# Kernel optimization log

Hardware: AMD Instinct MI355X
Metric: run time of the kernel (lower is better)

## Reference

```python
import jax, jax.numpy as jnp
import numpy as np
import math

B, T, D_IN, D_OUT = 4, 2048, 2048, 2048

def _inv_sigmoid(v):
    return math.log(v / (1 - v + 1e-08))

def setup_inputs() -> dict:
    key = jax.random.key(0)
    ks = jax.random.split(key, 6)
    x = jax.random.normal(ks[0], (B, T, D_IN), dtype=jnp.float32)
    W_p = jax.random.normal(ks[1], (D_OUT, D_IN), dtype=jnp.float32) * 0.02
    W_i = jax.random.normal(ks[2], (D_OUT, D_IN), dtype=jnp.float32) * 0.002
    W_d = jax.random.normal(ks[3], (D_OUT, D_IN), dtype=jnp.float32) * 0.002
    alpha_logit = jnp.full((D_IN,), _inv_sigmoid(0.9), dtype=jnp.float32)
    beta_logit = jnp.full((D_IN,), _inv_sigmoid(0.5), dtype=jnp.float32)
    W_gate_w = jax.random.normal(ks[4], (3, 3 * D_IN), dtype=jnp.float32) * 0.01
    W_gate_b = jnp.array([1.0, 0.0, 0.0], dtype=jnp.float32)
    bias = jnp.zeros((D_OUT,), dtype=jnp.float32)
    return {"x": x, "W_p": W_p, "W_i": W_i, "W_d": W_d,
            "alpha_logit": alpha_logit, "beta_logit": beta_logit,
            "W_gate_w": W_gate_w, "W_gate_b": W_gate_b, "bias": bias}

def _pid_features(x, alpha, beta):
    # x: (B,T,D). Single scan computing EMA integral and smoothed derivative.
    x_t = jnp.swapaxes(x, 0, 1)  # (T,B,D)
    x_prev = jnp.concatenate([jnp.zeros_like(x_t[:1]), x_t[:-1]], axis=0)
    diff_t = x_t - x_prev  # raw finite difference
    def step(carry, inp):
        s, d = carry
        xt, dt = inp
        s = alpha * s + (1.0 - alpha) * xt
        d = beta * d + (1.0 - beta) * dt
        return (s, d), (s, d)
    s0 = jnp.zeros(x.shape[::2], dtype=x.dtype)  # (B,D)
    _, (integ_t, deriv_t) = jax.lax.scan(step, (s0, s0), (x_t, diff_t))
    return jnp.swapaxes(integ_t, 0, 1), jnp.swapaxes(deriv_t, 0, 1)

def reference(x, W_p, W_i, W_d, alpha_logit, beta_logit, W_gate_w, W_gate_b, bias):
    alpha = jax.nn.sigmoid(alpha_logit)  # (D,)
    beta = jax.nn.sigmoid(beta_logit)
    integral, derivative = _pid_features(x, alpha, beta)  # (B,T,D) each
    gate_in = jnp.concatenate([x, integral, derivative], axis=-1)  # (B,T,3D)
    logits = jnp.einsum('btk,gk->btg', gate_in, W_gate_w) + W_gate_b
    gates = jax.nn.softmax(logits, axis=-1)  # (B,T,3)
    p_out = jnp.einsum('btd,od->bto', x, W_p)
    i_out = jnp.einsum('btd,od->bto', integral, W_i)
    d_out = jnp.einsum('btd,od->bto', derivative, W_d)
    y = gates[..., 0:1] * p_out + gates[..., 1:2] * i_out + gates[..., 2:3] * d_out + bias
    return y
```

## Files before the change

kernel.cpp:

```cpp
#include <hip/hip_runtime.h>
#include <stdint.h>

typedef unsigned short u16;

#define GAS __attribute__((address_space(1)))
#define LAS __attribute__((address_space(3)))

typedef __bf16 bf16x8 __attribute__((ext_vector_type(8)));
typedef float f32x4 __attribute__((ext_vector_type(4)));


__device__ inline u16 f2b(float f) {
    uint32_t x = __float_as_uint(f);
    uint32_t r = (x + 0x7fffu + ((x >> 16) & 1u)) >> 16;
    return (u16)r;
}

__device__ inline float b2f(u16 u) {
    union { uint32_t i; float f; } v;
    v.i = ((uint32_t)u) << 16;
    return v.f;
}

__device__ inline void load8b(float* v, const u16* p) {
    uint4 u = *(const uint4*)p;
    v[0] = b2f((u16)(u.x)); v[1] = b2f((u16)(u.x >> 16));
    v[2] = b2f((u16)(u.y)); v[3] = b2f((u16)(u.y >> 16));
    v[4] = b2f((u16)(u.z)); v[5] = b2f((u16)(u.z >> 16));
    v[6] = b2f((u16)(u.w)); v[7] = b2f((u16)(u.w >> 16));
}

__device__ inline void load8f(float* v, const float* p) {
    float4 a = *(const float4*)p;
    float4 b = *(const float4*)(p + 4);
    v[0] = a.x; v[1] = a.y; v[2] = a.z; v[3] = a.w;
    v[4] = b.x; v[5] = b.y; v[6] = b.z; v[7] = b.w;
}

__device__ inline void store8b(u16* p, const float* v, float scale) {
    uint4 u;
    u.x = (uint32_t)f2b(v[0] * scale) | ((uint32_t)f2b(v[1] * scale) << 16);
    u.y = (uint32_t)f2b(v[2] * scale) | ((uint32_t)f2b(v[3] * scale) << 16);
    u.z = (uint32_t)f2b(v[4] * scale) | ((uint32_t)f2b(v[5] * scale) << 16);
    u.w = (uint32_t)f2b(v[6] * scale) | ((uint32_t)f2b(v[7] * scale) << 16);
    *(uint4*)p = u;
}

__device__ inline float sigmoidf(float v) { return 1.f / (1.f + __expf(-v)); }

__device__ inline float pow64f(float a) {
    float p = a * a;
    p = p * p;
    p = p * p;
    p = p * p;
    p = p * p;
    return p * p;
}

__device__ inline float* carry_ptr(u16* Z, int plane, int b, int c, int d) {
    int f = ((plane * 4 + b) * 32 + c) * 2048 + d;
    int row = f >> 10;
    int off = f & 1023;
    return (float*)(Z + (size_t)row * 6144) + off;
}

__global__ __launch_bounds__(256) void pack_w(
    const float* __restrict__ Wp, const float* __restrict__ Wi,
    const float* __restrict__ Wd, u16* __restrict__ Wcat)
{
    int i = (blockIdx.x * 256 + threadIdx.x) * 8;
    int seg = i >> 22;
    int j = i & 4194303;
    const float* src = (seg == 0) ? Wp : (seg == 1) ? Wi : Wd;
    int o = j >> 11;
    int c = j & 2047;
    float v[8];
    load8f(v, src + j);
    store8b(Wcat + (size_t)o * 6144 + seg * 2048 + c, v, 1.0f);
}

__global__ __launch_bounds__(256) void scan_pass1(
    const float* __restrict__ x, const float* __restrict__ alog,
    const float* __restrict__ blog, u16* __restrict__ Z)
{
    const int d = blockIdx.x * 256 + threadIdx.x;
    const int c = blockIdx.y;
    const int b = blockIdx.z;
    const float alpha = sigmoidf(alog[d]);
    const float beta  = sigmoidf(blog[d]);
    const float oma = 1.f - alpha, omb = 1.f - beta;
    const float* xp = x + ((size_t)b * 2048 + c * 64) * 2048 + d;
    float xprev = (c == 0) ? 0.f : xp[-2048];
    float s = 0.f, dd = 0.f;
    #pragma unroll 8
    for (int t = 0; t < 64; ++t) {
        float xf = xp[(size_t)t * 2048];
        s = alpha * s + oma * xf;
        dd = beta * dd + omb * (xf - xprev);
        xprev = xf;
    }
    *carry_ptr(Z, 0, b, c, d) = s;
    *carry_ptr(Z, 1, b, c, d) = dd;
}

__global__ __launch_bounds__(256) void scan_pass2(
    const float* __restrict__ alog, const float* __restrict__ blog,
    u16* __restrict__ Z)
{
    const int g = blockIdx.x * 256 + threadIdx.x;
    const int b = g >> 11;
    const int d = g & 2047;
    const float aL = pow64f(sigmoidf(alog[d]));
    const float bL = pow64f(sigmoidf(blog[d]));
    float sIn = 0.f, dIn = 0.f;
    for (int c = 0; c < 32; ++c) {
        float* sp = carry_ptr(Z, 0, b, c, d);
        float* dp = carry_ptr(Z, 1, b, c, d);
        float sl = *sp, dl = *dp;
        *sp = sIn; *dp = dIn;
        sIn = sl + aL * sIn;
        dIn = dl + bL * dIn;
    }
}

__global__ __launch_bounds__(256) void scan_pass3(
    const float* __restrict__ x, const float* __restrict__ alog,
    const float* __restrict__ blog, u16* __restrict__ Z)
{
    const int d = blockIdx.x * 256 + threadIdx.x;
    const int c = blockIdx.y;
    const int b = blockIdx.z;
    const float alpha = sigmoidf(alog[d]);
    const float beta  = sigmoidf(blog[d]);
    const float oma = 1.f - alpha, omb = 1.f - beta;
    const float* xp = x + ((size_t)b * 2048 + c * 64) * 2048 + d;
    u16* zp = Z + ((size_t)b * 2048 + c * 64) * 6144 + 2048 + d;
    float s  = *carry_ptr(Z, 0, b, c, d);
    float dd = *carry_ptr(Z, 1, b, c, d);
    float xprev = (c == 0) ? 0.f : xp[-2048];
    #pragma unroll 8
    for (int t = 0; t < 64; ++t) {
        float xf = xp[(size_t)t * 2048];
        s = alpha * s + oma * xf;
        dd = beta * dd + omb * (xf - xprev);
        xprev = xf;
        size_t zo = (size_t)t * 6144;
        zp[zo] = f2b(s);
        zp[zo + 2048] = f2b(dd);
    }
}

__global__ __launch_bounds__(256) void gates_kernel(
    const float* __restrict__ x, const float* __restrict__ Wg,
    const float* __restrict__ Wgb, u16* __restrict__ Z)
{
    const int row = blockIdx.x;
    const int tid = threadIdx.x;
    const int k = tid * 8;
    const float* xr = x + (size_t)row * 2048;
    u16* zr = Z + (size_t)row * 6144;

    float xv[8], sv[8], dv[8];
    load8f(xv, xr + k);
    load8b(sv, zr + 2048 + k);
    load8b(dv, zr + 4096 + k);

    float p[3];
    #pragma unroll
    for (int gg = 0; gg < 3; ++gg) {
        float wx[8], ws[8], wd[8];
        load8f(wx, Wg + gg * 6144 + k);
        load8f(ws, Wg + gg * 6144 + 2048 + k);
        load8f(wd, Wg + gg * 6144 + 4096 + k);
        float acc = 0.f;
        #pragma unroll
        for (int j = 0; j < 8; ++j)
            acc += xv[j] * wx[j] + sv[j] * ws[j] + dv[j] * wd[j];
        p[gg] = acc;
    }

    #pragma unroll
    for (int off = 32; off > 0; off >>= 1) {
        p[0] += __shfl_down(p[0], off);
        p[1] += __shfl_down(p[1], off);
        p[2] += __shfl_down(p[2], off);
    }

    __shared__ float red[4][3];
    __shared__ float gsh[3];
    int wv = tid >> 6, lane = tid & 63;
    if (lane == 0) { red[wv][0] = p[0]; red[wv][1] = p[1]; red[wv][2] = p[2]; }
    __syncthreads();
    if (tid == 0) {
        float l0 = red[0][0] + red[1][0] + red[2][0] + red[3][0] + Wgb[0];
        float l1 = red[0][1] + red[1][1] + red[2][1] + red[3][1] + Wgb[1];
        float l2 = red[0][2] + red[1][2] + red[2][2] + red[3][2] + Wgb[2];
        float m = fmaxf(l0, fmaxf(l1, l2));
        float e0 = __expf(l0 - m), e1 = __expf(l1 - m), e2 = __expf(l2 - m);
        float inv = 1.f / (e0 + e1 + e2);
        gsh[0] = e0 * inv; gsh[1] = e1 * inv; gsh[2] = e2 * inv;
    }
    __syncthreads();
    float g0 = gsh[0], g1 = gsh[1], g2 = gsh[2];
    store8b(zr + k, xv, g0);
    store8b(zr + 2048 + k, sv, g1);
    store8b(zr + 4096 + k, dv, g2);
}

__global__ __launch_bounds__(512, 2) void gemm_kernel(
    const u16* __restrict__ Z, const u16* __restrict__ Wcat,
    const float* __restrict__ bias, float* __restrict__ out)
{
    extern __shared__ u16 lds[];
    u16* const lA = lds;
    u16* const lB = lds + 32768;

    const int tid = threadIdx.x;
    const int bn = blockIdx.x * 256;
    const int bm = blockIdx.y * 256;

    const int srow = tid >> 2;
    const int sgg  = (tid & 3) ^ ((tid >> 2) & 3) ^ ((tid >> 4) & 3);
    const u16* aglob = Z    + (size_t)(bm + srow) * 6144 + sgg * 8;
    const u16* bglob = Wcat + (size_t)(bn + srow) * 6144 + sgg * 8;

    const int lane = tid & 63;
    const int wv = tid >> 6;
    const int wm = wv & 1;
    const int wn = wv >> 1;
    const int fr = lane & 15;
    const int fq = lane >> 4;
    const int g  = fq ^ ((fr ^ (fr >> 2)) & 3);
    const int aoff = (wm * 128 + fr) * 32 + g * 8;
    const int boff = (wn * 64 + fr) * 32 + g * 8;

    f32x4 acc[8][4] = {};

#define XSTAGE(L, Gp, jt, h) do {                                             \
    u16* d_ = (L) + (((h) * 2 + ((jt) & 1)) * 8192) + tid * 8;                \
    const u16* s_ = (Gp) + (size_t)(jt) * 64 + (h) * 32;                      \
    __builtin_amdgcn_global_load_lds((const GAS uint32_t*)s_,                 \
                                     (LAS uint32_t*)d_, 16, 0, 0);            \
    __builtin_amdgcn_global_load_lds(                                         \
        (const GAS uint32_t*)(s_ + (size_t)128 * 6144),                       \
        (LAS uint32_t*)(d_ + 4096), 16, 0, 0);                                \
} while (0)

    XSTAGE(lA, aglob, 0, 0);
    XSTAGE(lB, bglob, 0, 0);
    XSTAGE(lA, aglob, 0, 1);
    XSTAGE(lB, bglob, 0, 1);
    XSTAGE(lA, aglob, 1, 0);
    XSTAGE(lB, bglob, 1, 0);
    asm volatile("s_waitcnt vmcnt(4)" ::: "memory");
    __builtin_amdgcn_s_barrier();

    for (int kt = 0; kt < 96; ++kt) {
        const int p = kt & 1;
        int t1 = kt + 1; if (t1 == 96) t1 = 0;
        int t2 = kt + 2; if (t2 >= 96) t2 -= 96;
        const u16* aLo = lA + (0 * 2 + p) * 8192;
        const u16* bLo = lB + (0 * 2 + p) * 8192;
        const u16* aHi = lA + (2 + p) * 8192;
        const u16* bHi = lB + (2 + p) * 8192;

        bf16x8 av[4], bv[4];

        #pragma unroll
        for (int i = 0; i < 4; ++i) av[i] = *(const bf16x8*)(aLo + aoff + i * 512);
        #pragma unroll
        for (int j = 0; j < 4; ++j) bv[j] = *(const bf16x8*)(bLo + boff + j * 512);
        XSTAGE(lA, aglob, t1, 1);
        __builtin_amdgcn_s_barrier();
        __builtin_amdgcn_s_setprio(1);
        #pragma unroll
        for (int i = 0; i < 4; ++i)
            #pragma unroll
            for (int j = 0; j < 4; ++j)
                acc[i][j] = __builtin_amdgcn_mfma_f32_16x16x32_bf16(
                    av[i], bv[j], acc[i][j], 0, 0, 0);
        __builtin_amdgcn_s_setprio(0);
        __builtin_amdgcn_s_barrier();

        #pragma unroll
        for (int i = 0; i < 4; ++i)
            av[i] = *(const bf16x8*)(aLo + aoff + (4 + i) * 512);
        XSTAGE(lB, bglob, t1, 1);
        __builtin_amdgcn_s_barrier();
        __builtin_amdgcn_s_setprio(1);
        #pragma unroll
        for (int i = 0; i < 4; ++i)
            #pragma unroll
            for (int j = 0; j < 4; ++j)
                acc[4 + i][j] = __builtin_amdgcn_mfma_f32_16x16x32_bf16(
                    av[i], bv[j], acc[4 + i][j], 0, 0, 0);
        __builtin_amdgcn_s_setprio(0);
        __builtin_amdgcn_s_barrier();

        #pragma unroll
        for (int i = 0; i < 4; ++i) av[i] = *(const bf16x8*)(aHi + aoff + i * 512);
        #pragma unroll
        for (int j = 0; j < 4; ++j) bv[j] = *(const bf16x8*)(bHi + boff + j * 512);
        XSTAGE(lA, aglob, t2, 0);
        __builtin_amdgcn_s_barrier();
        __builtin_amdgcn_s_setprio(1);
        #pragma unroll
        for (int i = 0; i < 4; ++i)
            #pragma unroll
            for (int j = 0; j < 4; ++j)
                acc[i][j] = __builtin_amdgcn_mfma_f32_16x16x32_bf16(
                    av[i], bv[j], acc[i][j], 0, 0, 0);
        __builtin_amdgcn_s_setprio(0);
        __builtin_amdgcn_s_barrier();

        #pragma unroll
        for (int i = 0; i < 4; ++i)
            av[i] = *(const bf16x8*)(aHi + aoff + (4 + i) * 512);
        XSTAGE(lB, bglob, t2, 0);
        __builtin_amdgcn_s_barrier();
        __builtin_amdgcn_s_setprio(1);
        #pragma unroll
        for (int i = 0; i < 4; ++i)
            #pragma unroll
            for (int j = 0; j < 4; ++j)
                acc[4 + i][j] = __builtin_amdgcn_mfma_f32_16x16x32_bf16(
                    av[i], bv[j], acc[4 + i][j], 0, 0, 0);
        __builtin_amdgcn_s_setprio(0);
        asm volatile("s_waitcnt vmcnt(4)" ::: "memory");
        __builtin_amdgcn_s_barrier();
    }

    asm volatile("s_waitcnt vmcnt(0)" ::: "memory");

    #pragma unroll
    for (int j = 0; j < 4; ++j) {
        const int col = bn + wn * 64 + j * 16 + fr;
        const float bb = bias[col];
        #pragma unroll
        for (int mf = 0; mf < 8; ++mf) {
            const int row0 = bm + wm * 128 + mf * 16 + fq * 4;
            #pragma unroll
            for (int r = 0; r < 4; ++r)
                out[(size_t)(row0 + r) * 2048 + col] = acc[mf][j][r] + bb;
        }
    }
#undef XSTAGE
}

extern "C" void kernel_launch(void* const* d_in, const int* in_sizes, int n_in,
                              void* d_out, int out_size, void* d_ws, size_t ws_size,
                              hipStream_t stream) {
    const float* x    = (const float*)d_in[0];
    const float* Wp   = (const float*)d_in[1];
    const float* Wi   = (const float*)d_in[2];
    const float* Wd   = (const float*)d_in[3];
    const float* al   = (const float*)d_in[4];
    const float* bl   = (const float*)d_in[5];
    const float* Wg   = (const float*)d_in[6];
    const float* Wgb  = (const float*)d_in[7];
    const float* bias = (const float*)d_in[8];
    float* out = (float*)d_out;

    u16* Z    = (u16*)d_ws;
    u16* Wcat = (u16*)((char*)d_ws + (size_t)8192 * 6144 * 2);

    static bool lds_cfgd = false;
    if (!lds_cfgd) {
        (void)hipFuncSetAttribute((const void*)gemm_kernel,
                                  hipFuncAttributeMaxDynamicSharedMemorySize,
                                  131072);
        lds_cfgd = true;
    }

    pack_w<<<6144, 256, 0, stream>>>(Wp, Wi, Wd, Wcat);
    scan_pass1<<<dim3(8, 32, 4), 256, 0, stream>>>(x, al, bl, Z);
    scan_pass2<<<32, 256, 0, stream>>>(al, bl, Z);
    scan_pass3<<<dim3(8, 32, 4), 256, 0, stream>>>(x, al, bl, Z);
    gates_kernel<<<8192, 256, 0, stream>>>(x, Wg, Wgb, Z);
    gemm_kernel<<<dim3(8, 32), 512, 131072, stream>>>(Z, Wcat, bias, out);
}
```

Baseline: 426.7 us.

## Restructure GEMM LDS staging to 64-wide K tiles with new swizzle

Changes the LDS tile layout from two 32-wide K halves to 64-element rows with an 8-way XOR swizzle. Each K-step now stages the full 64-wide K slice, split into row-quarter pieces, into a double buffer. The wait counts are adjusted so the next tile's global-to-LDS loads overlap the MFMA phases. This should cut bank conflicts and simplify the prefetch schedule, but the pipeline depth drops from two tiles ahead to one, which risks exposing memory latency. The last iteration redundantly reloads tile 95.

```diff
diff --git a/kernel.cpp b/kernel.cpp
--- a/kernel.cpp
+++ b/kernel.cpp
@@ -219,10 +219,10 @@
     const int bn = blockIdx.x * 256;
     const int bm = blockIdx.y * 256;
 
-    const int srow = tid >> 2;
-    const int sgg  = (tid & 3) ^ ((tid >> 2) & 3) ^ ((tid >> 4) & 3);
-    const u16* aglob = Z    + (size_t)(bm + srow) * 6144 + sgg * 8;
-    const u16* bglob = Wcat + (size_t)(bn + srow) * 6144 + sgg * 8;
+    const int sr  = tid >> 3;
+    const int scq = (tid & 7) ^ (sr & 7);
+    const u16* aglob = Z    + (size_t)(bm + sr) * 6144 + scq * 8;
+    const u16* bglob = Wcat + (size_t)(bn + sr) * 6144 + scq * 8;
 
     const int lane = tid & 63;
     const int wv = tid >> 6;
@@ -230,48 +230,46 @@
     const int wn = wv >> 1;
     const int fr = lane & 15;
     const int fq = lane >> 4;
-    const int g  = fq ^ ((fr ^ (fr >> 2)) & 3);
-    const int aoff = (wm * 128 + fr) * 32 + g * 8;
-    const int boff = (wn * 64 + fr) * 32 + g * 8;
+    const int chlo = fq ^ (fr & 7);
+    const int aoff = fr * 64 + chlo * 8;
+    const int boff = ((wn & 1) * 64 + fr) * 64 + chlo * 8;
+    const int aoffh = aoff ^ 32;
+    const int boffh = boff ^ 32;
 
     f32x4 acc[8][4] = {};
 
-#define XSTAGE(L, Gp, jt, h) do {                                             \
-    u16* d_ = (L) + (((h) * 2 + ((jt) & 1)) * 8192) + tid * 8;                \
-    const u16* s_ = (Gp) + (size_t)(jt) * 64 + (h) * 32;                      \
-    __builtin_amdgcn_global_load_lds((const GAS uint32_t*)s_,                 \
-                                     (LAS uint32_t*)d_, 16, 0, 0);            \
-    __builtin_amdgcn_global_load_lds(                                         \
-        (const GAS uint32_t*)(s_ + (size_t)128 * 6144),                       \
-        (LAS uint32_t*)(d_ + 4096), 16, 0, 0);                                \
-} while (0)
-
-    XSTAGE(lA, aglob, 0, 0);
-    XSTAGE(lB, bglob, 0, 0);
-    XSTAGE(lA, aglob, 0, 1);
-    XSTAGE(lB, bglob, 0, 1);
-    XSTAGE(lA, aglob, 1, 0);
-    XSTAGE(lB, bglob, 1, 0);
-    asm volatile("s_waitcnt vmcnt(4)" ::: "memory");
+#define GLOAD(gsrc, ldst)                                                     \
+    __builtin_amdgcn_global_load_lds((const GAS uint32_t*)(gsrc),             \
+                                     (LAS uint32_t*)(ldst), 16, 0, 0)
+
+    GLOAD(bglob,                        lB + tid * 8);
+    GLOAD(bglob + (size_t) 64 * 6144,   lB + 4096 + tid * 8);
+    GLOAD(bglob + (size_t)128 * 6144,   lB + 8192 + tid * 8);
+    GLOAD(bglob + (size_t)192 * 6144,   lB + 8192 + 4096 + tid * 8);
+    GLOAD(aglob,                        lA + tid * 8);
+    GLOAD(aglob + (size_t)128 * 6144,   lA + 8192 + tid * 8);
+    GLOAD(aglob + (size_t) 64 * 6144,   lA + 4096 + tid * 8);
+    GLOAD(aglob + (size_t)192 * 6144,   lA + 8192 + 4096 + tid * 8);
+    asm volatile("s_waitcnt vmcnt(2)" ::: "memory");
     __builtin_amdgcn_s_barrier();
 
     for (int kt = 0; kt < 96; ++kt) {
-        const int p = kt & 1;
-        int t1 = kt + 1; if (t1 == 96) t1 = 0;
-        int t2 = kt + 2; if (t2 >= 96) t2 -= 96;
-        const u16* aLo = lA + (0 * 2 + p) * 8192;
-        const u16* bLo = lB + (0 * 2 + p) * 8192;
-        const u16* aHi = lA + (2 + p) * 8192;
-        const u16* bHi = lB + (2 + p) * 8192;
-
+        const int pb  = (kt & 1) * 2;
+        const int nbb = pb ^ 2;
+        const int t1  = (kt < 95) ? kt + 1 : 95;
+        const size_t kc = (size_t)t1 * 64;
+        const u16* aS = lA + (pb + wm) * 8192;
+        const u16* bS = lB + (pb + (wn >> 1)) * 8192;
         bf16x8 av[4], bv[4];
 
         #pragma unroll
-        for (int i = 0; i < 4; ++i) av[i] = *(const bf16x8*)(aLo + aoff + i * 512);
-        #pragma unroll
-        for (int j = 0; j < 4; ++j) bv[j] = *(const bf16x8*)(bLo + boff + j * 512);
-        XSTAGE(lA, aglob, t1, 1);
-        __builtin_amdgcn_s_barrier();
+        for (int i = 0; i < 4; ++i) av[i] = *(const bf16x8*)(aS + aoff + i * 1024);
+        #pragma unroll
+        for (int j = 0; j < 4; ++j) bv[j] = *(const bf16x8*)(bS + boff + j * 1024);
+        GLOAD(bglob + kc,                      lB + nbb * 8192 + tid * 8);
+        GLOAD(bglob + (size_t)64 * 6144 + kc,  lB + nbb * 8192 + 4096 + tid * 8);
+        __builtin_amdgcn_s_barrier();
+        asm volatile("s_waitcnt lgkmcnt(0)" ::: "memory");
         __builtin_amdgcn_s_setprio(1);
         #pragma unroll
         for (int i = 0; i < 4; ++i)
@@ -280,13 +278,16 @@
                 acc[i][j] = __builtin_amdgcn_mfma_f32_16x16x32_bf16(
                     av[i], bv[j], acc[i][j], 0, 0, 0);
         __builtin_amdgcn_s_setprio(0);
-        __builtin_amdgcn_s_barrier();
-
-        #pragma unroll
-        for (int i = 0; i < 4; ++i)
-            av[i] = *(const bf16x8*)(aLo + aoff + (4 + i) * 512);
-        XSTAGE(lB, bglob, t1, 1);
-        __builtin_amdgcn_s_barrier();
+        asm volatile("s_waitcnt vmcnt(2)" ::: "memory");
+        __builtin_amdgcn_s_barrier();
+
+        #pragma unroll
+        for (int i = 0; i < 4; ++i)
+            av[i] = *(const bf16x8*)(aS + aoff + 4096 + i * 1024);
+        GLOAD(bglob + (size_t)128 * 6144 + kc, lB + (nbb + 1) * 8192 + tid * 8);
+        GLOAD(bglob + (size_t)192 * 6144 + kc, lB + (nbb + 1) * 8192 + 4096 + tid * 8);
+        __builtin_amdgcn_s_barrier();
+        asm volatile("s_waitcnt lgkmcnt(0)" ::: "memory");
         __builtin_amdgcn_s_setprio(1);
         #pragma unroll
         for (int i = 0; i < 4; ++i)
@@ -298,11 +299,13 @@
         __builtin_amdgcn_s_barrier();
 
         #pragma unroll
-        for (int i = 0; i < 4; ++i) av[i] = *(const bf16x8*)(aHi + aoff + i * 512);
-        #pragma unroll
-        for (int j = 0; j < 4; ++j) bv[j] = *(const bf16x8*)(bHi + boff + j * 512);
-        XSTAGE(lA, aglob, t2, 0);
-        __builtin_amdgcn_s_barrier();
+        for (int i = 0; i < 4; ++i) av[i] = *(const bf16x8*)(aS + aoffh + i * 1024);
+        #pragma unroll
+        for (int j = 0; j < 4; ++j) bv[j] = *(const bf16x8*)(bS + boffh + j * 1024);
+        GLOAD(aglob + kc,                      lA + nbb * 8192 + tid * 8);
+        GLOAD(aglob + (size_t)128 * 6144 + kc, lA + (nbb + 1) * 8192 + tid * 8);
+        __builtin_amdgcn_s_barrier();
+        asm volatile("s_waitcnt lgkmcnt(0)" ::: "memory");
         __builtin_amdgcn_s_setprio(1);
         #pragma unroll
         for (int i = 0; i < 4; ++i)
@@ -315,9 +318,11 @@
 
         #pragma unroll
         for (int i = 0; i < 4; ++i)
-            av[i] = *(const bf16x8*)(aHi + aoff + (4 + i) * 512);
-        XSTAGE(lB, bglob, t2, 0);
-        __builtin_amdgcn_s_barrier();
+            av[i] = *(const bf16x8*)(aS + aoffh + 4096 + i * 1024);
+        GLOAD(aglob + (size_t) 64 * 6144 + kc, lA + nbb * 8192 + 4096 + tid * 8);
+        GLOAD(aglob + (size_t)192 * 6144 + kc, lA + (nbb + 1) * 8192 + 4096 + tid * 8);
+        __builtin_amdgcn_s_barrier();
+        asm volatile("s_waitcnt lgkmcnt(0)" ::: "memory");
         __builtin_amdgcn_s_setprio(1);
         #pragma unroll
         for (int i = 0; i < 4; ++i)
@@ -326,7 +331,7 @@
                 acc[4 + i][j] = __builtin_amdgcn_mfma_f32_16x16x32_bf16(
                     av[i], bv[j], acc[4 + i][j], 0, 0, 0);
         __builtin_amdgcn_s_setprio(0);
-        asm volatile("s_waitcnt vmcnt(4)" ::: "memory");
+        asm volatile("s_waitcnt vmcnt(2)" ::: "memory");
         __builtin_amdgcn_s_barrier();
     }
 
@@ -344,7 +349,7 @@
                 out[(size_t)(row0 + r) * 2048 + col] = acc[mf][j][r] + bb;
         }
     }
-#undef XSTAGE
+#undef GLOAD
 }
 
 extern "C" void kernel_launch(void* const* d_in, const int* in_sizes, int n_in,
```

New measurement: 413.7 us. 1.03x faster.
